# Kernel optimization log

Hardware: AMD Instinct MI355X
Metric: run time of the kernel (lower is better)

Reference implementation:

```python
import jax, jax.numpy as jnp
import numpy as np

H, W, C, UP = 32, 32, 1024, 2  # num_patch=(32,32), embed_dim=1024, upsample_rate=2


def setup_inputs() -> dict:
    key = jax.random.key(0)
    k1, k2 = jax.random.split(key)
    x = jax.random.normal(k1, (32, H * W, C), dtype=jnp.float32)
    # keras Conv2D 1x1 kernel (1,1,Cin,Cout) squeezed to (Cin, Cout); Cin = Cout = C//UP
    w = jax.random.normal(k2, (C // UP, C // UP), dtype=jnp.float32) * 0.02
    return {"x": x, "w": w}


def reference(x, w):
    B, L, Cin = x.shape
    assert L == H * W and Cin == C
    xg = x.reshape(B, H, W, C)
    x0 = xg[..., : C // UP]        # [B,H,W,C/2]
    x1 = xg[..., C // UP:]         # [B,H,W,C/2]
    # Row-wise interleave: output rows alternate x0[i], x1[i] -> [B, 2H, W, C/2]
    xi = jnp.stack([x0, x1], axis=2).reshape(B, 2 * H, W, C // UP)
    # 1x1 conv (no bias) == per-pixel linear projection C/2 -> C/2
    y = jnp.einsum('bhwc,cd->bhwd', xi, w)
    # return_vector=True: tokens [B, 2L, C//2]
    return y.reshape(B, L * UP, C // 2)
```

## Files before the change

### kernel.cpp

```cpp
#include <hip/hip_runtime.h>
#include <hip/hip_bf16.h>
#include <stdint.h>

typedef __attribute__((ext_vector_type(4))) float f32x4;
typedef __attribute__((ext_vector_type(16))) float f32x16;
typedef __attribute__((ext_vector_type(8))) short bf16x8;
typedef __attribute__((ext_vector_type(4))) uint32_t u32x4;

#define KD 512
#define ND 512

__device__ __forceinline__ uint32_t pk_bf16(float lo, float hi) {
  uint32_t ulo = __float_as_uint(lo) + 0x8000u;
  uint32_t uhi = __float_as_uint(hi) + 0x8000u;
  return __builtin_amdgcn_perm(uhi, ulo, 0x07060302u);
}

__global__ void wt_kernel(const float* __restrict__ w, uint16_t* __restrict__ wt) {
  __shared__ float tile[32][33];
  const int bx = blockIdx.x, by = blockIdx.y;
  const int tx = threadIdx.x, ty = threadIdx.y;
#pragma unroll
  for (int i = 0; i < 32; i += 8)
    tile[ty + i][tx] = w[(bx * 32 + ty + i) * ND + by * 32 + tx];
  __syncthreads();
#pragma unroll
  for (int i = 0; i < 32; i += 8) {
    uint32_t u = __float_as_uint(tile[tx][ty + i]);
    uint32_t r = (u + 0x7FFFu + ((u >> 16) & 1u)) >> 16;
    wt[(by * 32 + ty + i) * KD + bx * 32 + tx] = (uint16_t)r;
  }
}

__global__ __launch_bounds__(256, 2) void gemm_kernel(
    const float* __restrict__ x, const uint16_t* __restrict__ wt,
    float* __restrict__ out) {
  __shared__ uint16_t As[64 * 512];

  const int tid = threadIdx.x;
  const int lane = tid & 63;
  const int l31 = lane & 31, hi = lane >> 5;
  const int wid = tid >> 6;
  const int m0 = blockIdx.x * 64;

  {
    const int r = tid >> 2;
    const int c0 = tid & 3;
    const int aRow = m0 + ((r & 31) << 1) + (r >> 5);
    const char* src = (const char*)x + (size_t)aRow * (KD * 4) + c0 * 32;
    char* dst = (char*)As + r * 1024;
    const int rx = (r & 7) << 1;
#pragma unroll 8
    for (int i = 0; i < 16; ++i) {
      const int c = c0 + i * 4;
      f32x4 lo = *(const f32x4*)(src + i * 128);
      f32x4 h4 = *(const f32x4*)(src + i * 128 + 16);
      u32x4 p = {pk_bf16(lo.x, lo.y), pk_bf16(lo.z, lo.w),
                 pk_bf16(h4.x, h4.y), pk_bf16(h4.z, h4.w)};
      *(u32x4*)(dst + (c ^ rx) * 16) = p;
    }
  }
  __syncthreads();

  const char* wb = (const char*)wt;
  uint32_t aBase[2], aXor[2];
#pragma unroll
  for (int rg = 0; rg < 2; ++rg) {
    const int u = rg * 32 + l31;
    aBase[rg] = u * 1024;
    aXor[rg] = (u & 7) << 1;
  }

#pragma unroll 1
  for (int cg = 0; cg < 4; ++cg) {
    const uint32_t col = (uint32_t)(cg * 128 + wid * 32 + l31);
    const char* wp = wb + col * (KD * 2) + hi * 16;
    bf16x8 wreg[32];
#pragma unroll
    for (int ks = 0; ks < 32; ++ks)
      wreg[ks] = *(const bf16x8*)(wp + ks * 32);

#pragma unroll
    for (int rg = 0; rg < 2; ++rg) {
      f32x16 acc;
#pragma unroll
      for (int e = 0; e < 16; ++e) acc[e] = 0.f;
#pragma unroll
      for (int ks = 0; ks < 32; ++ks) {
        const uint32_t s = (uint32_t)(2 * ks + hi) ^ aXor[rg];
        bf16x8 af = *(const bf16x8*)((const char*)As + aBase[rg] + s * 16);
        acc = __builtin_amdgcn_mfma_f32_32x32x16_bf16(wreg[ks], af, acc, 0, 0, 0);
      }
      float* op = out + (size_t)(m0 + rg * 32 + l31) * ND + cg * 128 + wid * 32;
#pragma unroll
      for (int q = 0; q < 4; ++q) {
        f32x4 v = {acc[q * 4 + 0], acc[q * 4 + 1],
                   acc[q * 4 + 2], acc[q * 4 + 3]};
        *(f32x4*)(op + q * 8 + hi * 4) = v;
      }
    }
  }
}

extern "C" void kernel_launch(void* const* d_in, const int* in_sizes, int n_in,
                              void* d_out, int out_size, void* d_ws, size_t ws_size,
                              hipStream_t stream) {
  const float* x = (const float*)d_in[0];
  const float* w = (const float*)d_in[1];
  float* out = (float*)d_out;
  uint16_t* wt = (uint16_t*)d_ws;

  wt_kernel<<<dim3(16, 16), dim3(32, 8), 0, stream>>>(w, wt);
  gemm_kernel<<<dim3(1024), dim3(256), 0, stream>>>(x, wt, out);
}
```

Measured before the change: 318.2 us.

## Use 512-thread blocks with 2x2 MFMA tiles per wave and pipelined weight loads

Doubles the block to 8 waves. Each wave now owns a 64-column slab and computes a 2x2 grid of 32x32 MFMA tiles in a single k-loop, instead of looping over four column groups with a full 32-register weight preload each time. Weight fragments are streamed through a 4-deep register ring prefetched 3 steps ahead, which cuts register pressure and lets each A fragment from LDS feed two MFMAs. The staging loop is split across twice as many threads. The risk is exposed global-load latency on the weight stream and higher occupancy demands from launch_bounds(512,4) against the 64 KB LDS tile.

```diff
diff --git a/kernel.cpp b/kernel.cpp
--- a/kernel.cpp
+++ b/kernel.cpp
@@ -32,7 +32,7 @@
   }
 }
 
-__global__ __launch_bounds__(256, 2) void gemm_kernel(
+__global__ __launch_bounds__(512, 4) void gemm_kernel(
     const float* __restrict__ x, const uint16_t* __restrict__ wt,
     float* __restrict__ out) {
   __shared__ uint16_t As[64 * 512];
@@ -44,17 +44,17 @@
   const int m0 = blockIdx.x * 64;
 
   {
-    const int r = tid >> 2;
-    const int c0 = tid & 3;
+    const int r = tid >> 3;
+    const int c0 = tid & 7;
     const int aRow = m0 + ((r & 31) << 1) + (r >> 5);
     const char* src = (const char*)x + (size_t)aRow * (KD * 4) + c0 * 32;
     char* dst = (char*)As + r * 1024;
     const int rx = (r & 7) << 1;
-#pragma unroll 8
-    for (int i = 0; i < 16; ++i) {
-      const int c = c0 + i * 4;
-      f32x4 lo = *(const f32x4*)(src + i * 128);
-      f32x4 h4 = *(const f32x4*)(src + i * 128 + 16);
+#pragma unroll
+    for (int i = 0; i < 8; ++i) {
+      const int c = c0 + i * 8;
+      f32x4 lo = *(const f32x4*)(src + i * 256);
+      f32x4 h4 = *(const f32x4*)(src + i * 256 + 16);
       u32x4 p = {pk_bf16(lo.x, lo.y), pk_bf16(lo.z, lo.w),
                  pk_bf16(h4.x, h4.y), pk_bf16(h4.z, h4.w)};
       *(u32x4*)(dst + (c ^ rx) * 16) = p;
@@ -63,40 +63,63 @@
   __syncthreads();
 
   const char* wb = (const char*)wt;
-  uint32_t aBase[2], aXor[2];
+  uint32_t wOff[2];
+#pragma unroll
+  for (int tn = 0; tn < 2; ++tn)
+    wOff[tn] = (uint32_t)(wid * 64 + tn * 32 + l31) * (KD * 2) + hi * 16;
+
+  const uint32_t ax = (l31 & 7) << 1;
+  uint32_t aBase[2];
+#pragma unroll
+  for (int rg = 0; rg < 2; ++rg) aBase[rg] = (rg * 32 + l31) * 1024;
+
+  f32x16 acc[2][2];
+#pragma unroll
+  for (int rg = 0; rg < 2; ++rg)
+#pragma unroll
+    for (int tn = 0; tn < 2; ++tn)
+#pragma unroll
+      for (int e = 0; e < 16; ++e) acc[rg][tn][e] = 0.f;
+
+  bf16x8 wf[4][2];
+#pragma unroll
+  for (int ks = 0; ks < 3; ++ks)
+#pragma unroll
+    for (int tn = 0; tn < 2; ++tn)
+      wf[ks][tn] = *(const bf16x8*)(wb + wOff[tn] + ks * 32);
+
+#pragma unroll
+  for (int ks = 0; ks < 32; ++ks) {
+    if (ks + 3 < 32) {
+#pragma unroll
+      for (int tn = 0; tn < 2; ++tn)
+        wf[(ks + 3) & 3][tn] =
+            *(const bf16x8*)(wb + wOff[tn] + (ks + 3) * 32);
+    }
+    bf16x8 af[2];
+#pragma unroll
+    for (int rg = 0; rg < 2; ++rg) {
+      const uint32_t s = (uint32_t)(2 * ks + hi) ^ ax;
+      af[rg] = *(const bf16x8*)((const char*)As + aBase[rg] + s * 16);
+    }
+#pragma unroll
+    for (int rg = 0; rg < 2; ++rg)
+#pragma unroll
+      for (int tn = 0; tn < 2; ++tn)
+        acc[rg][tn] = __builtin_amdgcn_mfma_f32_32x32x16_bf16(
+            wf[ks & 3][tn], af[rg], acc[rg][tn], 0, 0, 0);
+  }
+
 #pragma unroll
   for (int rg = 0; rg < 2; ++rg) {
-    const int u = rg * 32 + l31;
-    aBase[rg] = u * 1024;
-    aXor[rg] = (u & 7) << 1;
-  }
-
-#pragma unroll 1
-  for (int cg = 0; cg < 4; ++cg) {
-    const uint32_t col = (uint32_t)(cg * 128 + wid * 32 + l31);
-    const char* wp = wb + col * (KD * 2) + hi * 16;
-    bf16x8 wreg[32];
+    float* op = out + (size_t)(m0 + rg * 32 + l31) * ND + wid * 64;
 #pragma unroll
-    for (int ks = 0; ks < 32; ++ks)
-      wreg[ks] = *(const bf16x8*)(wp + ks * 32);
-
-#pragma unroll
-    for (int rg = 0; rg < 2; ++rg) {
-      f32x16 acc;
-#pragma unroll
-      for (int e = 0; e < 16; ++e) acc[e] = 0.f;
-#pragma unroll
-      for (int ks = 0; ks < 32; ++ks) {
-        const uint32_t s = (uint32_t)(2 * ks + hi) ^ aXor[rg];
-        bf16x8 af = *(const bf16x8*)((const char*)As + aBase[rg] + s * 16);
-        acc = __builtin_amdgcn_mfma_f32_32x32x16_bf16(wreg[ks], af, acc, 0, 0, 0);
-      }
-      float* op = out + (size_t)(m0 + rg * 32 + l31) * ND + cg * 128 + wid * 32;
+    for (int tn = 0; tn < 2; ++tn) {
 #pragma unroll
       for (int q = 0; q < 4; ++q) {
-        f32x4 v = {acc[q * 4 + 0], acc[q * 4 + 1],
-                   acc[q * 4 + 2], acc[q * 4 + 3]};
-        *(f32x4*)(op + q * 8 + hi * 4) = v;
+        f32x4 v = {acc[rg][tn][q * 4 + 0], acc[rg][tn][q * 4 + 1],
+                   acc[rg][tn][q * 4 + 2], acc[rg][tn][q * 4 + 3]};
+        *(f32x4*)(op + tn * 32 + q * 8 + hi * 4) = v;
       }
     }
   }
@@ -111,5 +134,5 @@
   uint16_t* wt = (uint16_t*)d_ws;
 
   wt_kernel<<<dim3(16, 16), dim3(32, 8), 0, stream>>>(w, wt);
-  gemm_kernel<<<dim3(1024), dim3(256), 0, stream>>>(x, wt, out);
+  gemm_kernel<<<dim3(1024), dim3(512), 0, stream>>>(x, wt, out);
 }
```

New measurement: 293.5 us. 1.08x faster.
